# Kernel optimization log

Hardware: AMD Instinct MI355X
Metric: run time of the kernel (lower is better)

## Reference

```python
import jax, jax.numpy as jnp
import numpy as np

N_ADAPTERS = 64
RANK = 64
ALPHA = 1.0
SCALING = ALPHA / RANK


def setup_inputs() -> dict:
    key = jax.random.key(0)
    k1, k2, k3, k4 = jax.random.split(key, 4)
    x = jax.random.normal(k1, (16, 2048, 4096), dtype=jnp.float32)
    adapter_ids = jax.random.randint(k2, (16,), 0, N_ADAPTERS, dtype=jnp.int64)
    # A init: randn * 0.02 (as in module). B is zeros in the module init, but we
    # use small random values so the reference exercises nontrivial math.
    A = jax.random.normal(k3, (N_ADAPTERS, 4096, RANK), dtype=jnp.float32) * 0.02
    B = jax.random.normal(k4, (N_ADAPTERS, RANK, 4096), dtype=jnp.float32) * 0.02
    return {"x": x, "adapter_ids": adapter_ids, "A": A, "B": B}


def reference(x, adapter_ids, A, B):
    # Gather per-sample low-rank factors: [b, r, in], [b, out, r]
    B_req = B[adapter_ids]
    A_req = A[adapter_ids]
    # Bx: [b, n, r]
    Bx = jnp.einsum('bni,bri->bnr', x, B_req)
    # out: [b, n, out]
    out = jnp.einsum('bnr,bor->bno', Bx, A_req)
    return out * SCALING
```

## Files before the change

### kernel.cpp

```cpp
#include <hip/hip_runtime.h>
#include <hip/hip_bf16.h>


typedef __bf16 bf16x8 __attribute__((ext_vector_type(8)));
typedef float  f32x4  __attribute__((ext_vector_type(4)));

#define SEQLEN  2048
#define D_IN    4096
#define D_OUT   4096
#define RNK     64
#define TN      32
#define BK      128
#define NKB     (D_IN / BK)
#define BKP     136
#define BXP     72

__device__ __forceinline__ bf16x8 cvt8(f32x4 a, f32x4 b) {
    bf16x8 r;
    r[0] = (__bf16)a[0]; r[1] = (__bf16)a[1]; r[2] = (__bf16)a[2]; r[3] = (__bf16)a[3];
    r[4] = (__bf16)b[0]; r[5] = (__bf16)b[1]; r[6] = (__bf16)b[2]; r[7] = (__bf16)b[3];
    return r;
}

__global__ __launch_bounds__(256, 4) void lora_fused(
    const float* __restrict__ x, const int* __restrict__ ids,
    const float* __restrict__ A, const float* __restrict__ Bw,
    float* __restrict__ out)
{
    __shared__ __bf16 xs[2][TN * BKP];
    __shared__ __bf16 bxs[TN * BXP];

    const int tid  = threadIdx.x;
    const int wave = tid >> 6;
    const int lane = tid & 63;
    const int l15  = lane & 15;
    const int quad = lane >> 4;

    const int blk  = blockIdx.x;
    const int slot = blk >> 3;
    const int b    = (blk & 7) * 2 + (slot >> 6);
    const int nt   = slot & 63;

    const int aid = ids[b];
    const float* xb = x   + ((size_t)b * SEQLEN + (size_t)nt * TN) * D_IN;
    float*       ob = out + ((size_t)b * SEQLEN + (size_t)nt * TN) * D_OUT;
    const float* Aq = A  + (size_t)aid * D_OUT * RNK;
    const float* Bq = Bw + (size_t)aid * RNK * D_IN;

    f32x4 zero; zero[0] = zero[1] = zero[2] = zero[3] = 0.0f;

    f32x4 acc[2];
    acc[0] = zero; acc[1] = zero;

    const int srow = tid >> 3;
    const int sq   = tid & 7;
    const float* xsrc = xb + (size_t)srow * D_IN + sq * 16;
    const float* bsrc = Bq + (size_t)(wave * 16 + l15) * D_IN + quad * 8;

    f32x4 pre[4];
    {
        #pragma unroll
        for (int i = 0; i < 4; ++i)
            pre[i] = __builtin_nontemporal_load((const f32x4*)(xsrc + i * 4));
        __bf16* xd = &xs[0][srow * BKP + sq * 16];
        *(bf16x8*)xd       = cvt8(pre[0], pre[1]);
        *(bf16x8*)(xd + 8) = cvt8(pre[2], pre[3]);
    }

    for (int kb = 0; kb < NKB; ++kb) {
        if (kb + 1 < NKB) {
            const float* sp = xsrc + (size_t)(kb + 1) * BK;
            #pragma unroll
            for (int i = 0; i < 4; ++i)
                pre[i] = __builtin_nontemporal_load((const f32x4*)(sp + i * 4));
        }
        asm volatile("s_waitcnt lgkmcnt(0)\n\ts_barrier" ::: "memory");

        const float* bp = bsrc + (size_t)kb * BK;
        const __bf16* xc = xs[kb & 1];
        #pragma unroll
        for (int s = 0; s < 4; ++s) {
            f32x4 b0 = *(const f32x4*)(bp + s * 32);
            f32x4 b1 = *(const f32x4*)(bp + s * 32 + 4);
            bf16x8 bfrag = cvt8(b0, b1);
            #pragma unroll
            for (int t = 0; t < 2; ++t) {
                bf16x8 afrag = *(const bf16x8*)&xc[(t * 16 + l15) * BKP + s * 32 + quad * 8];
                acc[t] = __builtin_amdgcn_mfma_f32_16x16x32_bf16(afrag, bfrag, acc[t], 0, 0, 0);
            }
        }

        if (kb + 1 < NKB) {
            __bf16* xd = &xs[(kb + 1) & 1][srow * BKP + sq * 16];
            *(bf16x8*)xd       = cvt8(pre[0], pre[1]);
            *(bf16x8*)(xd + 8) = cvt8(pre[2], pre[3]);
        }
    }

    #pragma unroll
    for (int t = 0; t < 2; ++t)
        #pragma unroll
        for (int j = 0; j < 4; ++j)
            bxs[(t * 16 + quad * 4 + j) * BXP + wave * 16 + l15] =
                (__bf16)(acc[t][j] * 0.015625f);
    __syncthreads();

    bf16x8 a2[2][2];
    #pragma unroll
    for (int t = 0; t < 2; ++t)
        #pragma unroll
        for (int s = 0; s < 2; ++s)
            a2[t][s] = *(const bf16x8*)&bxs[(t * 16 + l15) * BXP + s * 32 + quad * 8];

    for (int oc = 0; oc < 16; ++oc) {
        const int o0 = oc * 256 + wave * 64;
        bf16x8 b2[4][2];
        #pragma unroll
        for (int ot = 0; ot < 4; ++ot) {
            const float* ap = Aq + (size_t)(o0 + ot * 16 + l15) * RNK + quad * 8;
            #pragma unroll
            for (int s = 0; s < 2; ++s) {
                f32x4 a0 = *(const f32x4*)(ap + s * 32);
                f32x4 a1 = *(const f32x4*)(ap + s * 32 + 4);
                b2[ot][s] = cvt8(a0, a1);
            }
        }
        f32x4 acc2[2][4];
        #pragma unroll
        for (int t = 0; t < 2; ++t)
            #pragma unroll
            for (int ot = 0; ot < 4; ++ot)
                acc2[t][ot] = zero;
        #pragma unroll
        for (int s = 0; s < 2; ++s)
            #pragma unroll
            for (int ot = 0; ot < 4; ++ot)
                #pragma unroll
                for (int t = 0; t < 2; ++t)
                    acc2[t][ot] = __builtin_amdgcn_mfma_f32_16x16x32_bf16(
                        a2[t][s], b2[ot][s], acc2[t][ot], 0, 0, 0);
        #pragma unroll
        for (int t = 0; t < 2; ++t)
            #pragma unroll
            for (int j = 0; j < 4; ++j)
                #pragma unroll
                for (int ot = 0; ot < 4; ++ot)
                    ob[(size_t)(t * 16 + quad * 4 + j) * D_OUT + o0 + ot * 16 + l15] =
                        acc2[t][ot][j];
    }
}

extern "C" void kernel_launch(void* const* d_in, const int* in_sizes, int n_in,
                              void* d_out, int out_size, void* d_ws, size_t ws_size,
                              hipStream_t stream) {
    (void)in_sizes; (void)n_in; (void)d_ws; (void)ws_size; (void)out_size;
    const float* x   = (const float*)d_in[0];
    const int*   ids = (const int*)d_in[1];
    const float* A   = (const float*)d_in[2];
    const float* B   = (const float*)d_in[3];
    float*       out = (float*)d_out;

    dim3 grid(1024), block(256);
    hipLaunchKernelGGL(lora_fused, grid, block, 0, stream, x, ids, A, B, out);
}
```

Measured before the change: 1.092 ms.

## Deepen stage-1 prefetch to two blocks and vectorize output stores via transposed MFMA

Stage 1 now prefetches x two K-blocks ahead with ping-pong register buffers and prefetches the B weight slice one block ahead, so global load latency can overlap the MFMAs. Stage 2 swaps the MFMA operands so each lane holds four consecutive output columns, which allows 16-byte vector stores instead of scalar strided stores. The cost is higher register pressure from the extra prefetch buffers, which could reduce occupancy under the 4-wave launch bound.

```diff
diff --git a/kernel.cpp b/kernel.cpp
--- a/kernel.cpp
+++ b/kernel.cpp
@@ -57,45 +57,67 @@
     const float* xsrc = xb + (size_t)srow * D_IN + sq * 16;
     const float* bsrc = Bq + (size_t)(wave * 16 + l15) * D_IN + quad * 8;
 
-    f32x4 pre[4];
+    f32x4 xpA[4], xpB[4];
+    f32x4 bpre[8];
+
+    #pragma unroll
+    for (int i = 0; i < 4; ++i)
+        xpA[i] = __builtin_nontemporal_load((const f32x4*)(xsrc + i * 4));
+    #pragma unroll
+    for (int i = 0; i < 4; ++i)
+        xpB[i] = __builtin_nontemporal_load((const f32x4*)(xsrc + BK + i * 4));
+    #pragma unroll
+    for (int s = 0; s < 4; ++s) {
+        bpre[2 * s]     = *(const f32x4*)(bsrc + s * 32);
+        bpre[2 * s + 1] = *(const f32x4*)(bsrc + s * 32 + 4);
+    }
     {
-        #pragma unroll
-        for (int i = 0; i < 4; ++i)
-            pre[i] = __builtin_nontemporal_load((const f32x4*)(xsrc + i * 4));
         __bf16* xd = &xs[0][srow * BKP + sq * 16];
-        *(bf16x8*)xd       = cvt8(pre[0], pre[1]);
-        *(bf16x8*)(xd + 8) = cvt8(pre[2], pre[3]);
+        *(bf16x8*)xd       = cvt8(xpA[0], xpA[1]);
+        *(bf16x8*)(xd + 8) = cvt8(xpA[2], xpA[3]);
     }
 
-    for (int kb = 0; kb < NKB; ++kb) {
-        if (kb + 1 < NKB) {
-            const float* sp = xsrc + (size_t)(kb + 1) * BK;
-            #pragma unroll
-            for (int i = 0; i < 4; ++i)
-                pre[i] = __builtin_nontemporal_load((const f32x4*)(sp + i * 4));
-        }
-        asm volatile("s_waitcnt lgkmcnt(0)\n\ts_barrier" ::: "memory");
+#define S1_STEP(KB, CUR, XPIN, XPOUT)                                          \
+    {                                                                          \
+        if ((KB) + 2 < NKB) {                                                  \
+            const float* sp_ = xsrc + (size_t)((KB) + 2) * BK;                 \
+            _Pragma("unroll")                                                  \
+            for (int i = 0; i < 4; ++i)                                        \
+                XPOUT[i] = __builtin_nontemporal_load((const f32x4*)(sp_ + i * 4)); \
+        }                                                                      \
+        bf16x8 bc_[4];      \
+        _Pragma("unroll")                                                      \
+        for (int s = 0; s < 4; ++s) bc_[s] = cvt8(bpre[2 * s], bpre[2 * s + 1]); \
+        if ((KB) + 1 < NKB) {                              \
+            const float* bp_ = bsrc + (size_t)((KB) + 1) * BK;                 \
+            _Pragma("unroll")                                                  \
+            for (int s = 0; s < 4; ++s) {                                      \
+                bpre[2 * s]     = *(const f32x4*)(bp_ + s * 32);               \
+                bpre[2 * s + 1] = *(const f32x4*)(bp_ + s * 32 + 4);           \
+            }                                                                  \
+        }                                                                      \
+        asm volatile("s_waitcnt lgkmcnt(0)\n\ts_barrier" ::: "memory");        \
+        const __bf16* xc_ = xs[CUR];                                           \
+        _Pragma("unroll")                                                      \
+        for (int s = 0; s < 4; ++s) {                                          \
+            _Pragma("unroll")                                                  \
+            for (int t = 0; t < 2; ++t) {                                      \
+                bf16x8 af_ = *(const bf16x8*)&xc_[(t * 16 + l15) * BKP + s * 32 + quad * 8]; \
+                acc[t] = __builtin_amdgcn_mfma_f32_16x16x32_bf16(af_, bc_[s], acc[t], 0, 0, 0); \
+            }                                                                  \
+        }                                                                      \
+        if ((KB) + 1 < NKB) {              \
+            __bf16* xd_ = &xs[(CUR) ^ 1][srow * BKP + sq * 16];                \
+            *(bf16x8*)xd_       = cvt8(XPIN[0], XPIN[1]);                      \
+            *(bf16x8*)(xd_ + 8) = cvt8(XPIN[2], XPIN[3]);                      \
+        }                                                                      \
+    }
 
-        const float* bp = bsrc + (size_t)kb * BK;
-        const __bf16* xc = xs[kb & 1];
-        #pragma unroll
-        for (int s = 0; s < 4; ++s) {
-            f32x4 b0 = *(const f32x4*)(bp + s * 32);
-            f32x4 b1 = *(const f32x4*)(bp + s * 32 + 4);
-            bf16x8 bfrag = cvt8(b0, b1);
-            #pragma unroll
-            for (int t = 0; t < 2; ++t) {
-                bf16x8 afrag = *(const bf16x8*)&xc[(t * 16 + l15) * BKP + s * 32 + quad * 8];
-                acc[t] = __builtin_amdgcn_mfma_f32_16x16x32_bf16(afrag, bfrag, acc[t], 0, 0, 0);
-            }
-        }
-
-        if (kb + 1 < NKB) {
-            __bf16* xd = &xs[(kb + 1) & 1][srow * BKP + sq * 16];
-            *(bf16x8*)xd       = cvt8(pre[0], pre[1]);
-            *(bf16x8*)(xd + 8) = cvt8(pre[2], pre[3]);
-        }
+    for (int kb = 0; kb < NKB; kb += 2) {
+        S1_STEP(kb,     0, xpB, xpA);
+        S1_STEP(kb + 1, 1, xpA, xpB);
     }
+#undef S1_STEP
 
     #pragma unroll
     for (int t = 0; t < 2; ++t)
@@ -125,28 +147,26 @@
                 b2[ot][s] = cvt8(a0, a1);
             }
         }
-        f32x4 acc2[2][4];
+        f32x4 acc2[4][2];
         #pragma unroll
-        for (int t = 0; t < 2; ++t)
+        for (int ot = 0; ot < 4; ++ot)
             #pragma unroll
-            for (int ot = 0; ot < 4; ++ot)
-                acc2[t][ot] = zero;
+            for (int t = 0; t < 2; ++t)
+                acc2[ot][t] = zero;
         #pragma unroll
         for (int s = 0; s < 2; ++s)
             #pragma unroll
             for (int ot = 0; ot < 4; ++ot)
                 #pragma unroll
                 for (int t = 0; t < 2; ++t)
-                    acc2[t][ot] = __builtin_amdgcn_mfma_f32_16x16x32_bf16(
-                        a2[t][s], b2[ot][s], acc2[t][ot], 0, 0, 0);
+                    acc2[ot][t] = __builtin_amdgcn_mfma_f32_16x16x32_bf16(
+                        b2[ot][s], a2[t][s], acc2[ot][t], 0, 0, 0);
         #pragma unroll
         for (int t = 0; t < 2; ++t)
             #pragma unroll
-            for (int j = 0; j < 4; ++j)
-                #pragma unroll
-                for (int ot = 0; ot < 4; ++ot)
-                    ob[(size_t)(t * 16 + quad * 4 + j) * D_OUT + o0 + ot * 16 + l15] =
-                        acc2[t][ot][j];
+            for (int ot = 0; ot < 4; ++ot)
+                *(f32x4*)(ob + (size_t)(t * 16 + l15) * D_OUT + o0 + ot * 16 + quad * 4) =
+                    acc2[ot][t];
     }
 }
 
```

After: 1.092 ms. No clear change (+0.0%).
